# Performance work log

Measured on AMD Instinct MI355X. Metric: run time of the kernel, lower is better.

## Reference

```python
import jax, jax.numpy as jnp
import numpy as np

B, L, H, NH, D, I = 2, 2048, 2048, 16, 128, 8192
EPS = 1e-6
ROPE_BASE = 10000.0


def rms_norm(x, w):
    x32 = x.astype(jnp.float32)
    n = x32 * jax.lax.rsqrt(jnp.mean(x32 * x32, axis=-1, keepdims=True) + EPS)
    return (n * w).astype(x.dtype)


def rope(x, offset):
    # x: [B, L, H, D], non-traditional (half-split) RoPE
    d = x.shape[-1]
    half = d // 2
    inv_freq = 1.0 / (ROPE_BASE ** (jnp.arange(half, dtype=jnp.float32) * 2.0 / d))
    pos = jnp.arange(x.shape[1], dtype=jnp.float32) + offset
    ang = pos[:, None] * inv_freq[None, :]              # [L, half]
    cos = jnp.cos(ang)[None, :, None, :]
    sin = jnp.sin(ang)[None, :, None, :]
    x1, x2 = x[..., :half], x[..., half:]
    out = jnp.concatenate([x1 * cos - x2 * sin, x2 * cos + x1 * sin], axis=-1)
    return out.astype(x.dtype)


def setup_inputs() -> dict:
    key = jax.random.key(0)
    ks = jax.random.split(key, 9)
    s = 0.02
    causal = jnp.where(jnp.tril(jnp.ones((L, L), dtype=bool)), 0.0, -1e9).astype(jnp.float32)
    return {
        "x": jax.random.normal(ks[0], (B, L, H), dtype=jnp.float32),
        "ln1_w": jnp.ones((H,), dtype=jnp.float32),
        "ln2_w": jnp.ones((H,), dtype=jnp.float32),
        "wq": jax.random.normal(ks[1], (H, H), dtype=jnp.float32) * s,
        "wk": jax.random.normal(ks[2], (H, H), dtype=jnp.float32) * s,
        "wv": jax.random.normal(ks[3], (H, H), dtype=jnp.float32) * s,
        "wo": jax.random.normal(ks[4], (H, H), dtype=jnp.float32) * s,
        "w_gate": jax.random.normal(ks[5], (I, H), dtype=jnp.float32) * s,
        "w_up": jax.random.normal(ks[6], (I, H), dtype=jnp.float32) * s,
        "w_down": jax.random.normal(ks[7], (H, I), dtype=jnp.float32) * s,
        "mask": causal,
        "offset": 0,
    }


def reference(x, ln1_w, ln2_w, wq, wk, wv, wo, w_gate, w_up, w_down, mask, offset):
    residual = x
    h = rms_norm(x, ln1_w)
    # QKV projections (torch Linear: y = x @ W.T)
    q = jnp.einsum("ble,oe->blo", h, wq).reshape(B, L, NH, D)
    k = jnp.einsum("ble,oe->blo", h, wk).reshape(B, L, NH, D)
    v = jnp.einsum("ble,oe->blo", h, wv).reshape(B, L, NH, D)
    q = rope(q, offset)
    k = rope(k, offset)
    # [B, NH, L, D]
    q = q.transpose(0, 2, 1, 3)
    k = k.transpose(0, 2, 1, 3)
    v = v.transpose(0, 2, 1, 3)
    scores = jnp.einsum("bhqd,bhkd->bhqk", q.astype(jnp.float32), k.astype(jnp.float32))
    scores = scores / np.sqrt(D).astype(np.float32)
    if mask is not None:
        scores = scores + mask
    probs = jax.nn.softmax(scores, axis=-1).astype(v.dtype)
    attn = jnp.einsum("bhqk,bhkd->bhqd", probs, v)
    attn = attn.transpose(0, 2, 1, 3).reshape(B, L, NH * D)
    h = jnp.einsum("blo,eo->ble", attn, wo)
    x = h + residual
    residual = x
    h = rms_norm(x, ln2_w)
    gate = jax.nn.silu(jnp.einsum("ble,ie->bli", h, w_gate))
    up = jnp.einsum("ble,ie->bli", h, w_up)
    mlp = jnp.einsum("bli,ei->ble", gate * up, w_down)
    return mlp + residual
```

## Files before the change

### kernel.cpp

```cpp
#include <hip/hip_runtime.h>
#include <stdint.h>

#define B_ 2
#define L_ 2048
#define H_ 2048
#define NH_ 16
#define D_ 128
#define I_ 8192
#define M_ (B_*L_)

typedef unsigned short u16;
typedef __attribute__((ext_vector_type(8))) short bf16x8;
typedef __attribute__((ext_vector_type(4))) float f32x4;

__device__ __forceinline__ u16 f2bf(float f) {
  union { float f; uint32_t u; } c; c.f = f;
  return (u16)((c.u + 0x7fffu + ((c.u >> 16) & 1u)) >> 16);
}
__device__ __forceinline__ float bf2f(u16 h) {
  union { uint32_t u; float f; } c; c.u = ((uint32_t)h) << 16;
  return c.f;
}
__device__ __forceinline__ void gload16(const void* g, void* l) {
  __builtin_amdgcn_global_load_lds(
      (__attribute__((address_space(1))) void*)g,
      (__attribute__((address_space(3))) void*)l, 16, 0, 0);
}

__global__ void cvt_w(const float* __restrict__ src, u16* __restrict__ dst, int n4) {
  int i = blockIdx.x * blockDim.x + threadIdx.x;
  if (i >= n4) return;
  float4 v = ((const float4*)src)[i];
  ushort4 o;
  o.x = f2bf(v.x); o.y = f2bf(v.y); o.z = f2bf(v.z); o.w = f2bf(v.w);
  ((ushort4*)dst)[i] = o;
}

__global__ __launch_bounds__(256) void down_reduce(const u16* __restrict__ p0,
                                                   const u16* __restrict__ p1,
                                                   const float* __restrict__ res,
                                                   float* __restrict__ out, int n4) {
  int i = blockIdx.x * blockDim.x + threadIdx.x;
  if (i >= n4) return;
  ushort4 a = ((const ushort4*)p0)[i];
  ushort4 b = ((const ushort4*)p1)[i];
  float4 r = ((const float4*)res)[i];
  float4 o;
  o.x = bf2f(a.x) + bf2f(b.x) + r.x;
  o.y = bf2f(a.y) + bf2f(b.y) + r.y;
  o.z = bf2f(a.z) + bf2f(b.z) + r.z;
  o.w = bf2f(a.w) + bf2f(b.w) + r.w;
  ((float4*)out)[i] = o;
}

__global__ __launch_bounds__(256) void rmsnorm_k(const float* __restrict__ x,
                                                 const float* __restrict__ w,
                                                 u16* __restrict__ out) {
  int row = blockIdx.x;
  int t = threadIdx.x;
  const float4* xr = (const float4*)(x + (size_t)row * H_);
  float4 a = xr[t * 2], b = xr[t * 2 + 1];
  float s = a.x*a.x + a.y*a.y + a.z*a.z + a.w*a.w
          + b.x*b.x + b.y*b.y + b.z*b.z + b.w*b.w;
  for (int m = 1; m < 64; m <<= 1) s += __shfl_xor(s, m);
  __shared__ float sm[4];
  if ((t & 63) == 0) sm[t >> 6] = s;
  __syncthreads();
  float tot = sm[0] + sm[1] + sm[2] + sm[3];
  float rs = rsqrtf(tot / (float)H_ + 1e-6f);
  const float4* wr = (const float4*)w;
  float4 w0 = wr[t * 2], w1 = wr[t * 2 + 1];
  ushort4 o0, o1;
  o0.x = f2bf(a.x * rs * w0.x); o0.y = f2bf(a.y * rs * w0.y);
  o0.z = f2bf(a.z * rs * w0.z); o0.w = f2bf(a.w * rs * w0.w);
  o1.x = f2bf(b.x * rs * w1.x); o1.y = f2bf(b.y * rs * w1.y);
  o1.z = f2bf(b.z * rs * w1.z); o1.w = f2bf(b.w * rs * w1.w);
  ushort4* orow = (ushort4*)(out + (size_t)row * H_);
  orow[t * 2] = o0; orow[t * 2 + 1] = o1;
}

__global__ void rope_tab(float* __restrict__ cosT, float* __restrict__ sinT,
                         const int* __restrict__ offp) {
  int i = blockIdx.x * blockDim.x + threadIdx.x;
  int d = i & 63, l = i >> 6;
  float inv = powf(10000.0f, -(float)d / 64.0f);
  float ang = (float)(l + *offp) * inv;
  cosT[i] = cosf(ang);
  sinT[i] = sinf(ang);
}

__global__ void rope_apply(u16* __restrict__ qk, const float* __restrict__ cosT,
                           const float* __restrict__ sinT) {
  int i = blockIdx.x * blockDim.x + threadIdx.x;
  int d = i & 63;
  size_t row = (size_t)(i >> 6);
  int l = (int)(row & (L_ - 1));
  u16* p = qk + row * D_;
  float x1 = bf2f(p[d]), x2 = bf2f(p[d + 64]);
  float c = cosT[l * 64 + d], s = sinT[l * 64 + d];
  p[d]      = f2bf(x1 * c - x2 * s);
  p[d + 64] = f2bf(x2 * c + x1 * s);
}

__global__ __launch_bounds__(256) void vtrans_k(const u16* __restrict__ v,
                                                u16* __restrict__ vt) {
  __shared__ u16 tile[64][65];
  int l0 = blockIdx.x * 64, d0 = blockIdx.y * 64;
  size_t base = (size_t)blockIdx.z * L_ * D_;
  int t = threadIdx.x;
  int tr = t >> 3, tc = (t & 7) * 8;
  #pragma unroll
  for (int it = 0; it < 2; ++it) {
    int r = tr + it * 32;
    const u16* src = v + base + (size_t)(l0 + r) * D_ + d0 + tc;
    ushort4 u0 = ((const ushort4*)src)[0], u1 = ((const ushort4*)src)[1];
    tile[r][tc + 0] = u0.x; tile[r][tc + 1] = u0.y;
    tile[r][tc + 2] = u0.z; tile[r][tc + 3] = u0.w;
    tile[r][tc + 4] = u1.x; tile[r][tc + 5] = u1.y;
    tile[r][tc + 6] = u1.z; tile[r][tc + 7] = u1.w;
  }
  __syncthreads();
  #pragma unroll
  for (int it = 0; it < 2; ++it) {
    int r = tr + it * 32;
    u16* dst = vt + base + (size_t)(d0 + r) * L_ + l0 + tc;
    ushort4 o0, o1;
    o0.x = tile[tc + 0][r]; o0.y = tile[tc + 1][r];
    o0.z = tile[tc + 2][r]; o0.w = tile[tc + 3][r];
    o1.x = tile[tc + 4][r]; o1.y = tile[tc + 5][r];
    o1.z = tile[tc + 6][r]; o1.w = tile[tc + 7][r];
    ((ushort4*)dst)[0] = o0; ((ushort4*)dst)[1] = o1;
  }
}

#define EPI_QKV 0
#define EPI_SILU 1
#define EPI_MUL 2
#define EPI_ADDRES 3
#define EPI_PART 4
#define EPI_QKV3 5

template <int EPI>
__global__ __launch_bounds__(256)
void gemm_bt(const u16* __restrict__ A, const u16* __restrict__ Bw,
             int M, int N, int K,
             u16* outb, float* outf, const float* __restrict__ resf) {
  __shared__ __attribute__((aligned(16))) u16 At[128 * 64];
  __shared__ __attribute__((aligned(16))) u16 Bt[128 * 64];
  int tid = threadIdx.x;
  int w = tid >> 6, lane = tid & 63;
  int r16 = lane & 15, g4 = lane >> 4;
  int wr = w >> 1, wc = w & 1;
  int m0 = blockIdx.y * 128;
  int n0 = blockIdx.x * 128;
  f32x4 acc[4][4] = {};
  const char* Ab = (const char*)A;
  const char* Bb = (const char*)Bw;
  int nk = K >> 6;
  for (int kt = 0; kt < nk; ++kt) {
    int k0 = kt << 6;
    #pragma unroll
    for (int i = 0; i < 4; ++i) {
      int uoff = i * 4096 + w * 1024;
      int lin = uoff + lane * 16;
      int row = lin >> 7;
      int colB = lin & 127;
      gload16(Ab + ((size_t)(m0 + row) * K + k0) * 2 + colB, (char*)At + uoff);
      gload16(Bb + ((size_t)(n0 + row) * K + k0) * 2 + colB, (char*)Bt + uoff);
    }
    __syncthreads();
    #pragma unroll
    for (int kk = 0; kk < 2; ++kk) {
      bf16x8 af[4], bfr[4];
      #pragma unroll
      for (int m = 0; m < 4; ++m)
        af[m] = *(const bf16x8*)&At[(wr * 64 + m * 16 + r16) * 64 + kk * 32 + g4 * 8];
      #pragma unroll
      for (int n = 0; n < 4; ++n)
        bfr[n] = *(const bf16x8*)&Bt[(wc * 64 + n * 16 + r16) * 64 + kk * 32 + g4 * 8];
      #pragma unroll
      for (int m = 0; m < 4; ++m)
        #pragma unroll
        for (int n = 0; n < 4; ++n)
          acc[m][n] = __builtin_amdgcn_mfma_f32_16x16x32_bf16(af[m], bfr[n], acc[m][n], 0, 0, 0);
    }
    __syncthreads();
  }
  #pragma unroll
  for (int m = 0; m < 4; ++m) {
    #pragma unroll
    for (int n = 0; n < 4; ++n) {
      #pragma unroll
      for (int r = 0; r < 4; ++r) {
        int row = m0 + wr * 64 + m * 16 + g4 * 4 + r;
        int col = n0 + wc * 64 + n * 16 + r16;
        float val = acc[m][n][r];
        if (EPI == EPI_QKV) {
          int b = row >> 11, l = row & 2047;
          int hh = col >> 7, d = col & 127;
          outb[((((size_t)b * NH_ + hh) * L_ + l) << 7) + d] = f2bf(val);
        } else if (EPI == EPI_SILU) {
          float sg = val / (1.0f + __expf(-val));
          outb[(size_t)row * N + col] = f2bf(sg);
        } else if (EPI == EPI_MUL) {
          float g = bf2f(outb[(size_t)row * N + col]);
          outb[(size_t)row * N + col] = f2bf(g * val);
        } else {
          outf[(size_t)row * N + col] = val + resf[(size_t)row * N + col];
        }
      }
    }
  }
}

template <int EPI>
__global__ __launch_bounds__(512, 2)
void gemm256(const u16* __restrict__ A, const u16* __restrict__ Bw,
             int M, int N, int K, int nk, int nslice,
             u16* __restrict__ outb, u16* __restrict__ outb2) {
  __shared__ __attribute__((aligned(16))) u16 Asm[2][2][8192];
  __shared__ __attribute__((aligned(16))) u16 Bsm[2][2][8192];
  int tid = threadIdx.x;
  int wid = tid >> 6, lane = tid & 63;
  int r16 = lane & 15, g4 = lane >> 4;
  int nwg = gridDim.x, bid = blockIdx.x;
  int q8 = nwg >> 3, r8 = nwg & 7, xcd = bid & 7, loc = bid >> 3;
  int wgall = (xcd < r8 ? xcd * (q8 + 1) : r8 * (q8 + 1) + (xcd - r8) * q8) + loc;
  int nwg_geo = (M >> 8) * (N >> 8);
  int ks = wgall / nwg_geo;
  int wg = wgall % nwg_geo;
  (void)nslice;
  int NX = N >> 8;
  int n0 = (wg % NX) * 256;
  int m0 = (wg / NX) * 256;
  const char* Ab = (const char*)(A + (size_t)ks * nk * 64);
  const char* Bb = (const char*)(Bw + (size_t)ks * nk * 64);
  u16* ob = (EPI == EPI_PART && ks) ? outb2 : outb;

  f32x4 acc[2][2][4][2] = {};
  bf16x8 afr[4][2];
  bf16x8 bfr[2][2][2];

  auto STAGE = [&](int kt1, int sel) {
    if (kt1 >= nk) return;
    int buf = kt1 & 1;
    int k0 = kt1 << 6;
    const char* gb; char* lb; int row0;
    if (sel == 0)      { gb = Ab; row0 = m0;       lb = (char*)&Asm[buf][0][0]; }
    else if (sel == 3) { gb = Ab; row0 = m0 + 128; lb = (char*)&Asm[buf][1][0]; }
    else if (sel == 1) { gb = Bb; row0 = n0;       lb = (char*)&Bsm[buf][0][0]; }
    else               { gb = Bb; row0 = n0 + 128; lb = (char*)&Bsm[buf][1][0]; }
    #pragma unroll
    for (int j = 0; j < 2; ++j) {
      int p = j * 8192 + wid * 1024 + lane * 16;
      int r = p >> 7;
      int cb = (p & 127) ^ ((r & 7) << 4);
      gload16(gb + ((size_t)(row0 + r) * K + k0) * 2 + cb,
              lb + j * 8192 + wid * 1024);
    }
  };

  STAGE(0, 0); STAGE(0, 1); STAGE(0, 2); STAGE(0, 3);

  const int QM[4] = {0, 0, 1, 1};
  const int QN[4] = {0, 1, 1, 0};

  for (int kt = 0; kt < nk; ++kt) {
    int cur = kt & 1;
    #pragma unroll
    for (int ph = 0; ph < 4; ++ph) {
      if (ph < 3) {
        __builtin_amdgcn_sched_barrier(0);
        asm volatile("s_waitcnt vmcnt(4)" ::: "memory");
      }
      __builtin_amdgcn_s_barrier();
      __builtin_amdgcn_sched_barrier(0);
      const int qm = QM[ph], qn = QN[ph];
      if (ph == 0 || ph == 2) {
        const char* Ah = (const char*)&Asm[cur][qm][0];
        #pragma unroll
        for (int mf = 0; mf < 4; ++mf) {
          int R = (wid >> 2) * 64 + mf * 16 + r16;
          int sw = (R & 7) << 4;
          afr[mf][0] = *(const bf16x8*)(Ah + R * 128 + ((g4 * 16) ^ sw));
          afr[mf][1] = *(const bf16x8*)(Ah + R * 128 + ((64 + g4 * 16) ^ sw));
        }
      }
      if (ph == 0 || ph == 1) {
        const char* Bh = (const char*)&Bsm[cur][qn][0];
        #pragma unroll
        for (int nf = 0; nf < 2; ++nf) {
          int R = (wid & 3) * 32 + nf * 16 + r16;
          int sw = (R & 7) << 4;
          bfr[qn][nf][0] = *(const bf16x8*)(Bh + R * 128 + ((g4 * 16) ^ sw));
          bfr[qn][nf][1] = *(const bf16x8*)(Bh + R * 128 + ((64 + g4 * 16) ^ sw));
        }
      }
      STAGE(kt + 1, ph);
      __builtin_amdgcn_s_setprio(1);
      #pragma unroll
      for (int mf = 0; mf < 4; ++mf)
        #pragma unroll
        for (int nf = 0; nf < 2; ++nf)
          #pragma unroll
          for (int kk = 0; kk < 2; ++kk)
            acc[qm][qn][mf][nf] = __builtin_amdgcn_mfma_f32_16x16x32_bf16(
                afr[mf][kk], bfr[qn][nf][kk], acc[qm][qn][mf][nf], 0, 0, 0);
      __builtin_amdgcn_s_setprio(0);
    }
  }
  #pragma unroll
  for (int qm = 0; qm < 2; ++qm)
    #pragma unroll
    for (int qn = 0; qn < 2; ++qn)
      #pragma unroll
      for (int mf = 0; mf < 4; ++mf)
        #pragma unroll
        for (int nf = 0; nf < 2; ++nf)
          #pragma unroll
          for (int rr = 0; rr < 4; ++rr) {
            int row = m0 + qm * 128 + (wid >> 2) * 64 + mf * 16 + g4 * 4 + rr;
            int col = n0 + qn * 128 + (wid & 3) * 32 + nf * 16 + r16;
            float val = acc[qm][qn][mf][nf][rr];
            if (EPI == EPI_SILU) {
              ob[(size_t)row * N + col] = f2bf(val / (1.0f + __expf(-val)));
            } else if (EPI == EPI_MUL) {
              float g = bf2f(ob[(size_t)row * N + col]);
              ob[(size_t)row * N + col] = f2bf(g * val);
            } else if (EPI == EPI_PART) {
              ob[(size_t)row * N + col] = f2bf(val);
            } else if (EPI == EPI_QKV3) {
              int which = col >> 11, within = col & 2047;
              int hh = within >> 7, d = within & 127;
              int bb = row >> 11, l = row & 2047;
              ob[(size_t)which * M_ * H_ +
                 ((((size_t)bb * NH_ + hh) * L_ + l) << 7) + d] = f2bf(val);
            }
          }
}

__global__ __launch_bounds__(256)
void flash_attn(const u16* __restrict__ q, const u16* __restrict__ k,
                const u16* __restrict__ vt, u16* __restrict__ out) {
  __shared__ __attribute__((aligned(16))) u16 Kt[64 * 128];
  __shared__ __attribute__((aligned(16))) u16 Vt[128 * 64];
  __shared__ __attribute__((aligned(16))) u16 Pl[4][16 * 64];
  int tid = threadIdx.x, w = tid >> 6, lane = tid & 63;
  int r16 = lane & 15, g4 = lane >> 4;
  int b = blockIdx.z, h = blockIdx.y;
  int qt = gridDim.x - 1 - blockIdx.x;
  int q0 = qt * 64;
  size_t bh = (size_t)b * NH_ + h;
  const char* qb = (const char*)(q + bh * L_ * D_);
  const char* kb = (const char*)(k + bh * L_ * D_);
  const char* vb = (const char*)(vt + bh * D_ * L_);
  int qrow = q0 + w * 16 + r16;
  bf16x8 qf[4];
  #pragma unroll
  for (int c = 0; c < 4; ++c)
    qf[c] = *(const bf16x8*)(qb + ((size_t)qrow * 128 + c * 32 + g4 * 8) * 2);
  f32x4 oacc[8] = {};
  float mrow[4], lsum[4];
  #pragma unroll
  for (int r = 0; r < 4; ++r) { mrow[r] = -3.0e38f; lsum[r] = 0.f; }
  int myq = q0 + w * 16 + g4 * 4;
  int ntiles = qt + 1;
  int rsw = (r16 & 7) << 4;
  const float sc = 0.08838834764831845f;
  for (int t = 0; t < ntiles; ++t) {
    int kv0 = t * 64;
    #pragma unroll
    for (int i = 0; i < 4; ++i) {
      int uoff = i * 4096 + w * 1024;
      int lin = uoff + lane * 16;
      int krow = lin >> 8;
      int kcol = (lin & 255) ^ ((krow & 7) << 4);
      gload16(kb + (size_t)(kv0 + krow) * 256 + kcol, (char*)Kt + uoff);
      int vrow = lin >> 7;
      int vcol = (lin & 127) ^ ((vrow & 7) << 4);
      gload16(vb + (size_t)vrow * (L_ * 2) + kv0 * 2 + vcol, (char*)Vt + uoff);
    }
    __syncthreads();
    f32x4 s[4] = {};
    __builtin_amdgcn_s_setprio(1);
    #pragma unroll
    for (int c = 0; c < 4; ++c) {
      #pragma unroll
      for (int n = 0; n < 4; ++n) {
        const char* kp = (const char*)Kt + (n * 16 + r16) * 256
                       + ((c * 64 + g4 * 16) ^ rsw);
        bf16x8 kf = *(const bf16x8*)kp;
        s[n] = __builtin_amdgcn_mfma_f32_16x16x32_bf16(qf[c], kf, s[n], 0, 0, 0);
      }
    }
    __builtin_amdgcn_s_setprio(0);
    #pragma unroll
    for (int r = 0; r < 4; ++r) {
      float rm = -3.0e38f;
      #pragma unroll
      for (int n = 0; n < 4; ++n) {
        float v = s[n][r] * sc;
        int kvi = kv0 + n * 16 + r16;
        if (kvi > myq + r) v = -3.0e38f;
        s[n][r] = v;
        rm = fmaxf(rm, v);
      }
      rm = fmaxf(rm, __shfl_xor(rm, 1));
      rm = fmaxf(rm, __shfl_xor(rm, 2));
      rm = fmaxf(rm, __shfl_xor(rm, 4));
      rm = fmaxf(rm, __shfl_xor(rm, 8));
      float mnew = fmaxf(mrow[r], rm);
      float alpha = __expf(mrow[r] - mnew);
      mrow[r] = mnew;
      lsum[r] *= alpha;
      #pragma unroll
      for (int nf = 0; nf < 8; ++nf) oacc[nf][r] *= alpha;
      int prow = g4 * 4 + r;
      int psw = (prow & 7) << 3;
      #pragma unroll
      for (int n = 0; n < 4; ++n) {
        float pv = __expf(s[n][r] - mnew);
        lsum[r] += pv;
        Pl[w][prow * 64 + ((n * 16 + r16) ^ psw)] = f2bf(pv);
      }
    }
    asm volatile("s_waitcnt lgkmcnt(0)" ::: "memory");
    __builtin_amdgcn_sched_barrier(0);
    __builtin_amdgcn_s_setprio(1);
    #pragma unroll
    for (int kc = 0; kc < 2; ++kc) {
      const char* pp = (const char*)&Pl[w][0] + r16 * 128
                     + ((kc * 64 + g4 * 16) ^ rsw);
      bf16x8 pf = *(const bf16x8*)pp;
      #pragma unroll
      for (int nf = 0; nf < 8; ++nf) {
        const char* vp = (const char*)Vt + (nf * 16 + r16) * 128
                       + ((kc * 64 + g4 * 16) ^ rsw);
        bf16x8 vf = *(const bf16x8*)vp;
        oacc[nf] = __builtin_amdgcn_mfma_f32_16x16x32_bf16(pf, vf, oacc[nf], 0, 0, 0);
      }
    }
    __builtin_amdgcn_s_setprio(0);
    __syncthreads();
  }
  #pragma unroll
  for (int r = 0; r < 4; ++r) {
    float l = lsum[r];
    l += __shfl_xor(l, 1); l += __shfl_xor(l, 2);
    l += __shfl_xor(l, 4); l += __shfl_xor(l, 8);
    float inv = 1.0f / l;
    size_t orow = ((size_t)b * L_ + (myq + r)) * H_ + h * D_;
    #pragma unroll
    for (int nf = 0; nf < 8; ++nf)
      out[orow + nf * 16 + r16] = f2bf(oacc[nf][r] * inv);
  }
}

extern "C" void kernel_launch(void* const* d_in, const int* in_sizes, int n_in,
                              void* d_out, int out_size, void* d_ws, size_t ws_size,
                              hipStream_t stream) {
  (void)in_sizes; (void)n_in; (void)out_size; (void)ws_size;
  const float* x    = (const float*)d_in[0];
  const float* ln1w = (const float*)d_in[1];
  const float* ln2w = (const float*)d_in[2];
  const float* wq   = (const float*)d_in[3];
  const float* wk   = (const float*)d_in[4];
  const float* wv   = (const float*)d_in[5];
  const float* wo   = (const float*)d_in[6];
  const float* wg   = (const float*)d_in[7];
  const float* wu   = (const float*)d_in[8];
  const float* wd   = (const float*)d_in[9];
  const int*   offp = (const int*)d_in[11];
  float* out = (float*)d_out;

  char* p = (char*)d_ws;
  auto alloc = [&](size_t bytes) {
    char* r = p;
    p += (bytes + 255) & ~(size_t)255;
    return r;
  };
  const size_t HH = (size_t)H_ * H_, IH = (size_t)I_ * H_;
  u16* wbuf = (u16*)alloc(IH * 2);
  u16* h1   = (u16*)alloc((size_t)M_ * H_ * 2);
  u16* qb   = (u16*)alloc((size_t)M_ * H_ * 2);
  u16* kb   = (u16*)alloc((size_t)M_ * H_ * 2);
  u16* vb   = (u16*)alloc((size_t)M_ * H_ * 2);
  u16* vtb  = (u16*)alloc((size_t)M_ * H_ * 2);
  u16* attn = (u16*)alloc((size_t)M_ * H_ * 2);
  float* x2 = (float*)alloc((size_t)M_ * H_ * 4);
  float* cosT = (float*)alloc((size_t)L_ * 64 * 4);
  float* sinT = (float*)alloc((size_t)L_ * 64 * 4);
  (void)kb; (void)vb;
  u16* h2    = h1;
  u16* gateb = qb;

  const int nHH4 = (int)(HH / 4), nIH4 = (int)(IH / 4);

  rmsnorm_k<<<M_, 256, 0, stream>>>(x, ln1w, h1);
  rope_tab<<<(L_ * 64) / 256, 256, 0, stream>>>(cosT, sinT, offp);

  cvt_w<<<nHH4 / 256, 256, 0, stream>>>(wq, wbuf, nHH4);
  cvt_w<<<nHH4 / 256, 256, 0, stream>>>(wk, wbuf + HH, nHH4);
  cvt_w<<<nHH4 / 256, 256, 0, stream>>>(wv, wbuf + 2 * HH, nHH4);
  int nwg_qkv = (M_ / 256) * (3 * H_ / 256);
  gemm256<EPI_QKV3><<<nwg_qkv, 512, 0, stream>>>(h1, wbuf, M_, 3 * H_, H_,
                                                 H_ / 64, 1, qb, nullptr);

  int nrope = B_ * NH_ * L_ * 64;
  rope_apply<<<nrope / 256, 256, 0, stream>>>(qb, cosT, sinT);
  rope_apply<<<nrope / 256, 256, 0, stream>>>(qb + (size_t)M_ * H_, cosT, sinT);
  vtrans_k<<<dim3(L_ / 64, D_ / 64, B_ * NH_), 256, 0, stream>>>(
      qb + 2 * (size_t)M_ * H_, vtb);

  flash_attn<<<dim3(L_ / 64, NH_, B_), 256, 0, stream>>>(
      qb, qb + (size_t)M_ * H_, vtb, attn);

  dim3 g1(H_ / 128, M_ / 128);
  cvt_w<<<nHH4 / 256, 256, 0, stream>>>(wo, wbuf, nHH4);
  gemm_bt<EPI_ADDRES><<<g1, 256, 0, stream>>>(attn, wbuf, M_, H_, H_, nullptr, x2, x);
  rmsnorm_k<<<M_, 256, 0, stream>>>(x2, ln2w, h2);

  int nwg256 = (M_ / 256) * (I_ / 256);
  cvt_w<<<nIH4 / 256, 256, 0, stream>>>(wg, wbuf, nIH4);
  gemm256<EPI_SILU><<<nwg256, 512, 0, stream>>>(h2, wbuf, M_, I_, H_,
                                                H_ / 64, 1, gateb, nullptr);
  cvt_w<<<nIH4 / 256, 256, 0, stream>>>(wu, wbuf, nIH4);
  gemm256<EPI_MUL><<<nwg256, 512, 0, stream>>>(h2, wbuf, M_, I_, H_,
                                               H_ / 64, 1, gateb, nullptr);

  cvt_w<<<nIH4 / 256, 256, 0, stream>>>(wd, wbuf, nIH4);
  int nwg_dn = 2 * (M_ / 256) * (H_ / 256);
  gemm256<EPI_PART><<<nwg_dn, 512, 0, stream>>>(gateb, wbuf, M_, H_, I_,
                                                I_ / 128, 2, h1, attn);
  down_reduce<<<(M_ * H_ / 4) / 256, 256, 0, stream>>>(h1, attn, x2, out,
                                                       M_ * H_ / 4);
}
```

Before: 868.9 us.

## Restructure gemm256 main loop into explicit four-phase LDS/MFMA pipeline

Replaces the unrolled phase loop in the 256x256 GEMM with an explicit sequence. Each quadrant now issues its LDS fragment reads and the next-tile global-to-LDS stage before the barrier, then waits on lgkmcnt before its MFMA block, and adds a second barrier after each MFMA group. The aim is to overlap LDS reads and global prefetch with the barrier wait and to order the phases more tightly. It adds barriers per k-step, which could increase synchronization cost. It also drops the unused nslice parameter.

```diff
diff --git a/kernel.cpp b/kernel.cpp
--- a/kernel.cpp
+++ b/kernel.cpp
@@ -216,7 +216,7 @@
 template <int EPI>
 __global__ __launch_bounds__(512, 2)
 void gemm256(const u16* __restrict__ A, const u16* __restrict__ Bw,
-             int M, int N, int K, int nk, int nslice,
+             int M, int N, int K, int nk,
              u16* __restrict__ outb, u16* __restrict__ outb2) {
   __shared__ __attribute__((aligned(16))) u16 Asm[2][2][8192];
   __shared__ __attribute__((aligned(16))) u16 Bsm[2][2][8192];
@@ -229,7 +229,6 @@
   int nwg_geo = (M >> 8) * (N >> 8);
   int ks = wgall / nwg_geo;
   int wg = wgall % nwg_geo;
-  (void)nslice;
   int NX = N >> 8;
   int n0 = (wg % NX) * 256;
   int m0 = (wg / NX) * 256;
@@ -259,55 +258,82 @@
               lb + j * 8192 + wid * 1024);
     }
   };
+  auto LDA = [&](int cur, int qm) {
+    const char* Ah = (const char*)&Asm[cur][qm][0];
+    #pragma unroll
+    for (int mf = 0; mf < 4; ++mf) {
+      int R = (wid >> 2) * 64 + mf * 16 + r16;
+      int sw = (R & 7) << 4;
+      afr[mf][0] = *(const bf16x8*)(Ah + R * 128 + ((g4 * 16) ^ sw));
+      afr[mf][1] = *(const bf16x8*)(Ah + R * 128 + ((64 + g4 * 16) ^ sw));
+    }
+  };
+  auto LDB = [&](int cur, int qn) {
+    const char* Bh = (const char*)&Bsm[cur][qn][0];
+    #pragma unroll
+    for (int nf = 0; nf < 2; ++nf) {
+      int R = (wid & 3) * 32 + nf * 16 + r16;
+      int sw = (R & 7) << 4;
+      bfr[qn][nf][0] = *(const bf16x8*)(Bh + R * 128 + ((g4 * 16) ^ sw));
+      bfr[qn][nf][1] = *(const bf16x8*)(Bh + R * 128 + ((64 + g4 * 16) ^ sw));
+    }
+  };
+  auto MFMA16 = [&](int qm, int qn) {
+    __builtin_amdgcn_s_setprio(1);
+    #pragma unroll
+    for (int mf = 0; mf < 4; ++mf)
+      #pragma unroll
+      for (int nf = 0; nf < 2; ++nf)
+        #pragma unroll
+        for (int kk = 0; kk < 2; ++kk)
+          acc[qm][qn][mf][nf] = __builtin_amdgcn_mfma_f32_16x16x32_bf16(
+              afr[mf][kk], bfr[qn][nf][kk], acc[qm][qn][mf][nf], 0, 0, 0);
+    __builtin_amdgcn_s_setprio(0);
+  };
 
   STAGE(0, 0); STAGE(0, 1); STAGE(0, 2); STAGE(0, 3);
-
-  const int QM[4] = {0, 0, 1, 1};
-  const int QN[4] = {0, 1, 1, 0};
+  asm volatile("s_waitcnt vmcnt(4)" ::: "memory");
+  __builtin_amdgcn_s_barrier();
 
   for (int kt = 0; kt < nk; ++kt) {
     int cur = kt & 1;
-    #pragma unroll
-    for (int ph = 0; ph < 4; ++ph) {
-      if (ph < 3) {
-        __builtin_amdgcn_sched_barrier(0);
-        asm volatile("s_waitcnt vmcnt(4)" ::: "memory");
-      }
-      __builtin_amdgcn_s_barrier();
-      __builtin_amdgcn_sched_barrier(0);
-      const int qm = QM[ph], qn = QN[ph];
-      if (ph == 0 || ph == 2) {
-        const char* Ah = (const char*)&Asm[cur][qm][0];
-        #pragma unroll
-        for (int mf = 0; mf < 4; ++mf) {
-          int R = (wid >> 2) * 64 + mf * 16 + r16;
-          int sw = (R & 7) << 4;
-          afr[mf][0] = *(const bf16x8*)(Ah + R * 128 + ((g4 * 16) ^ sw));
-          afr[mf][1] = *(const bf16x8*)(Ah + R * 128 + ((64 + g4 * 16) ^ sw));
-        }
-      }
-      if (ph == 0 || ph == 1) {
-        const char* Bh = (const char*)&Bsm[cur][qn][0];
-        #pragma unroll
-        for (int nf = 0; nf < 2; ++nf) {
-          int R = (wid & 3) * 32 + nf * 16 + r16;
-          int sw = (R & 7) << 4;
-          bfr[qn][nf][0] = *(const bf16x8*)(Bh + R * 128 + ((g4 * 16) ^ sw));
-          bfr[qn][nf][1] = *(const bf16x8*)(Bh + R * 128 + ((64 + g4 * 16) ^ sw));
-        }
-      }
-      STAGE(kt + 1, ph);
-      __builtin_amdgcn_s_setprio(1);
-      #pragma unroll
-      for (int mf = 0; mf < 4; ++mf)
-        #pragma unroll
-        for (int nf = 0; nf < 2; ++nf)
-          #pragma unroll
-          for (int kk = 0; kk < 2; ++kk)
-            acc[qm][qn][mf][nf] = __builtin_amdgcn_mfma_f32_16x16x32_bf16(
-                afr[mf][kk], bfr[qn][nf][kk], acc[qm][qn][mf][nf], 0, 0, 0);
-      __builtin_amdgcn_s_setprio(0);
-    }
+    LDA(cur, 0); LDB(cur, 0);
+    STAGE(kt + 1, 0);
+    __builtin_amdgcn_sched_barrier(0);
+    asm volatile("s_waitcnt vmcnt(4)" ::: "memory");
+    __builtin_amdgcn_s_barrier();
+    asm volatile("s_waitcnt lgkmcnt(0)" ::: "memory");
+    __builtin_amdgcn_sched_barrier(0);
+    MFMA16(0, 0);
+    __builtin_amdgcn_s_barrier();
+    __builtin_amdgcn_sched_barrier(0);
+    LDB(cur, 1);
+    STAGE(kt + 1, 1);
+    __builtin_amdgcn_sched_barrier(0);
+    asm volatile("s_waitcnt vmcnt(4)" ::: "memory");
+    __builtin_amdgcn_s_barrier();
+    asm volatile("s_waitcnt lgkmcnt(0)" ::: "memory");
+    __builtin_amdgcn_sched_barrier(0);
+    MFMA16(0, 1);
+    __builtin_amdgcn_s_barrier();
+    __builtin_amdgcn_sched_barrier(0);
+    LDA(cur, 1);
+    STAGE(kt + 1, 2);
+    __builtin_amdgcn_sched_barrier(0);
+    __builtin_amdgcn_s_barrier();
+    asm volatile("s_waitcnt lgkmcnt(0)" ::: "memory");
+    __builtin_amdgcn_sched_barrier(0);
+    MFMA16(1, 1);
+    __builtin_amdgcn_s_barrier();
+    __builtin_amdgcn_sched_barrier(0);
+    STAGE(kt + 1, 3);
+    __builtin_amdgcn_sched_barrier(0);
+    asm volatile("s_waitcnt vmcnt(4)" ::: "memory");
+    __builtin_amdgcn_s_barrier();
+    __builtin_amdgcn_sched_barrier(0);
+    MFMA16(1, 0);
+    __builtin_amdgcn_s_barrier();
+    __builtin_amdgcn_sched_barrier(0);
   }
   #pragma unroll
   for (int qm = 0; qm < 2; ++qm)
@@ -504,7 +530,7 @@
   cvt_w<<<nHH4 / 256, 256, 0, stream>>>(wv, wbuf + 2 * HH, nHH4);
   int nwg_qkv = (M_ / 256) * (3 * H_ / 256);
   gemm256<EPI_QKV3><<<nwg_qkv, 512, 0, stream>>>(h1, wbuf, M_, 3 * H_, H_,
-                                                 H_ / 64, 1, qb, nullptr);
+                                                 H_ / 64, qb, nullptr);
 
   int nrope = B_ * NH_ * L_ * 64;
   rope_apply<<<nrope / 256, 256, 0, stream>>>(qb, cosT, sinT);
@@ -523,15 +549,15 @@
   int nwg256 = (M_ / 256) * (I_ / 256);
   cvt_w<<<nIH4 / 256, 256, 0, stream>>>(wg, wbuf, nIH4);
   gemm256<EPI_SILU><<<nwg256, 512, 0, stream>>>(h2, wbuf, M_, I_, H_,
-                                                H_ / 64, 1, gateb, nullptr);
+                                                H_ / 64, gateb, nullptr);
   cvt_w<<<nIH4 / 256, 256, 0, stream>>>(wu, wbuf, nIH4);
   gemm256<EPI_MUL><<<nwg256, 512, 0, stream>>>(h2, wbuf, M_, I_, H_,
-                                               H_ / 64, 1, gateb, nullptr);
+                                               H_ / 64, gateb, nullptr);
 
   cvt_w<<<nIH4 / 256, 256, 0, stream>>>(wd, wbuf, nIH4);
   int nwg_dn = 2 * (M_ / 256) * (H_ / 256);
   gemm256<EPI_PART><<<nwg_dn, 512, 0, stream>>>(gateb, wbuf, M_, H_, I_,
-                                                I_ / 128, 2, h1, attn);
+                                                I_ / 128, h1, attn);
   down_reduce<<<(M_ * H_ / 4) / 256, 256, 0, stream>>>(h1, attn, x2, out,
                                                        M_ * H_ / 4);
 }
```

Result: slower. 902.2 us, median of 2 (+3.8%).
